# Performance work log

Measured on AMD Instinct MI355X. Metric: run time of the kernel, lower is better.

The kernel has to match this reference:

```python
import jax, jax.numpy as jnp
import numpy as np

N, E = 50000, 500000
HID, H, D = 128, 8, 16
ED, EGD = 32, 64


def _ln(x, g, b):
    m = x.mean(-1, keepdims=True)
    v = ((x - m) ** 2).mean(-1, keepdims=True)
    return (x - m) / jnp.sqrt(v + 1e-5) * g + b


def _gelu(x):
    return jax.nn.gelu(x, approximate=False)  # torch nn.GELU default (erf)


def setup_inputs() -> dict:
    key = jax.random.key(0)
    ks = jax.random.split(key, 24)
    s = lambda k, shape, scale=0.05: jax.random.normal(k, shape, jnp.float32) * scale
    inp = {
        "x": jax.random.normal(ks[0], (N, HID), jnp.float32),
        "edge_attr": jax.random.normal(ks[1], (E, ED), jnp.float32),
        "gamma": jax.random.uniform(ks[2], (N, HID), jnp.float32),
        "beta": jax.random.normal(ks[3], (N, HID), jnp.float32) * 0.1,
        "Wq": s(ks[4], (HID, H * D)),
        "Wk": s(ks[5], (HID, H * D)),
        "Wv": s(ks[6], (HID, H * D)),
        "Wo": s(ks[7], (H * D, HID)),
        "bo": jnp.zeros((HID,), jnp.float32),
        "ea_w1": s(ks[8], (ED, EGD)), "ea_b1": jnp.zeros((EGD,), jnp.float32),
        "ea_w2": s(ks[9], (EGD, H)), "ea_b2": jnp.zeros((H,), jnp.float32),
        "eg_w1": s(ks[10], (ED, EGD)), "eg_b1": jnp.zeros((EGD,), jnp.float32),
        "eg_w2": s(ks[11], (EGD, H * D)), "eg_b2": jnp.zeros((H * D,), jnp.float32),
        "ln1_g": jnp.ones((HID,), jnp.float32), "ln1_b": jnp.zeros((HID,), jnp.float32),
        "ln2_g": jnp.ones((HID,), jnp.float32), "ln2_b": jnp.zeros((HID,), jnp.float32),
        "ffn_w1": s(ks[12], (HID, 2 * HID)), "ffn_b1": jnp.zeros((2 * HID,), jnp.float32),
        "ffn_w2": s(ks[13], (2 * HID, HID)), "ffn_b2": jnp.zeros((HID,), jnp.float32),
        "edge_index": jax.random.randint(ks[14], (2, E), 0, N, jnp.int32),
    }
    return inp


def reference(x, edge_attr, gamma, beta, Wq, Wk, Wv, Wo, bo,
              ea_w1, ea_b1, ea_w2, ea_b2, eg_w1, eg_b1, eg_w2, eg_b2,
              ln1_g, ln1_b, ln2_g, ln2_b, ffn_w1, ffn_b1, ffn_w2, ffn_b2,
              edge_index):
    n = x.shape[0]
    src, dst = edge_index[0], edge_index[1]
    xn = _ln(x, ln1_g, ln1_b)
    Q = (xn @ Wq).reshape(n, H, D)
    K = (xn @ Wk).reshape(n, H, D)
    V = (xn @ Wv).reshape(n, H, D)
    # per-edge attention logits [E, H]
    logits = (Q[dst] * K[src]).sum(-1) * (D ** -0.5)
    logits = logits + (_gelu(edge_attr @ ea_w1 + ea_b1) @ ea_w2 + ea_b2)
    # sparse softmax over edges sharing a destination; torch version
    # initializes max buffer to zeros (include_self), so clamp max at 0
    m = jnp.maximum(jax.ops.segment_max(logits, dst, num_segments=n), 0.0)
    ex = jnp.exp(logits - m[dst])
    ssum = jax.ops.segment_sum(ex, dst, num_segments=n)
    attn = ex / (ssum[dst] + 1e-10)
    gate = jax.nn.sigmoid(_gelu(edge_attr @ eg_w1 + eg_b1) @ eg_w2 + eg_b2).reshape(-1, H, D)
    weighted = attn[..., None] * (gate * V[src])  # [E, H, D]
    agg = jax.ops.segment_sum(weighted, dst, num_segments=n).reshape(n, H * D)
    out = agg @ Wo + bo
    out = gamma * out + beta
    x = x + out
    x2 = _ln(x, ln2_g, ln2_b)
    f = _gelu(x2 @ ffn_w1 + ffn_b1) @ ffn_w2 + ffn_b2
    return x + f
```

## Files before the change

kernel.cpp:

```cpp
#include <hip/hip_runtime.h>

constexpr int N   = 50000;
constexpr int E   = 500000;
constexpr int HID = 128;
constexpr int NH  = 8;
constexpr int ED  = 32;
constexpr int EGD = 64;
constexpr int NB  = (N + 255) / 256;

typedef short  bf16x8 __attribute__((ext_vector_type(8)));
typedef float  f32x4  __attribute__((ext_vector_type(4)));

__device__ __forceinline__ float gelu_f(float v) {
    float u = v * v;
    float a = v * fmaf(u, -0.07135481283f, -1.5957691216f);
    float e = __expf(a);
    return v * __builtin_amdgcn_rcpf(1.f + e);
}
__device__ __forceinline__ float sigm_f(float v) {
    float e = __expf(-v);
    return __builtin_amdgcn_rcpf(1.f + e);
}
__device__ __forceinline__ unsigned short f2bf(float f) {
    unsigned int u = __float_as_uint(f);
    return (unsigned short)((u + 0x7fffu + ((u >> 16) & 1u)) >> 16);
}
__device__ __forceinline__ unsigned int cvt_pk_bf16(float lo, float hi) {
    unsigned int r;
    asm("v_cvt_pk_bf16_f32 %0, %1, %2" : "=v"(r) : "v"(lo), "v"(hi));
    return r;
}
__device__ __forceinline__ float dot2(unsigned int a, unsigned int b) {
    float al = __uint_as_float(a << 16), ah = __uint_as_float(a & 0xffff0000u);
    float bl = __uint_as_float(b << 16), bh = __uint_as_float(b & 0xffff0000u);
    return al * bl + ah * bh;
}

__global__ __launch_bounds__(256) void k_cvt(
    const float* __restrict__ Wq, const float* __restrict__ Wk,
    const float* __restrict__ Wv, const float* __restrict__ Wo,
    const float* __restrict__ fw1, const float* __restrict__ fw2,
    const float* __restrict__ ea_w1, const float* __restrict__ ea_w2,
    const float* __restrict__ eg_w1, const float* __restrict__ eg_w2,
    unsigned short* __restrict__ dst)
{
    int f = blockIdx.x * 256 + threadIdx.x;
    if (f >= 18048) return;
    const float* W; int KT, srcN, base;
    if      (f < 2048)  { W = Wq;    KT = 4; srcN = 128; base = 0; }
    else if (f < 4096)  { W = Wk;    KT = 4; srcN = 128; base = 2048; }
    else if (f < 6144)  { W = Wv;    KT = 4; srcN = 128; base = 4096; }
    else if (f < 8192)  { W = Wo;    KT = 4; srcN = 128; base = 6144; }
    else if (f < 12288) { W = fw1;   KT = 4; srcN = 256; base = 8192; }
    else if (f < 16384) { W = fw2;   KT = 8; srcN = 128; base = 12288; }
    else if (f < 16640) { W = ea_w1; KT = 1; srcN = 64;  base = 16384; }
    else if (f < 16768) { W = ea_w2; KT = 2; srcN = 8;   base = 16640; }
    else if (f < 17024) { W = eg_w1; KT = 1; srcN = 64;  base = 16768; }
    else                { W = eg_w2; KT = 2; srcN = 128; base = 17024; }
    int fl = f - base, lane = fl & 63, t = fl >> 6;
    int ks = t % KT, nt = t / KT;
    int n  = nt * 16 + (lane & 15);
    int k0 = ks * 32 + (lane >> 4) * 8;
    union { unsigned short u[8]; uint4 v; } o;
#pragma unroll
    for (int j = 0; j < 8; j++)
        o.u[j] = (n < srcN) ? f2bf(W[(size_t)(k0 + j) * srcN + n]) : (unsigned short)0;
    *(uint4*)(dst + (size_t)f * 8) = o.v;
}

__global__ __launch_bounds__(64) void k_ln_qkv_mfma(
    const float* __restrict__ x, const float* __restrict__ g1, const float* __restrict__ b1,
    const unsigned short* __restrict__ wqkv,
    unsigned short* __restrict__ Q, unsigned short* __restrict__ K, unsigned short* __restrict__ V)
{
    __shared__ unsigned short xn_lds[16 * 128];
    const int tid = threadIdx.x;
    const int nodeBase = blockIdx.x * 16;

    {
        int nl = tid >> 2, q = tid & 3;
        int gn = nodeBase + nl; if (gn >= N) gn = N - 1;
        const float4* xp = (const float4*)(x + (size_t)gn * HID + q * 32);
        float xv[32]; float s = 0.f, ss = 0.f;
#pragma unroll
        for (int i = 0; i < 8; i++) {
            float4 t = xp[i];
            xv[4*i] = t.x; xv[4*i+1] = t.y; xv[4*i+2] = t.z; xv[4*i+3] = t.w;
        }
#pragma unroll
        for (int i = 0; i < 32; i++) { s += xv[i]; ss += xv[i] * xv[i]; }
        s += __shfl_xor(s, 1); ss += __shfl_xor(ss, 1);
        s += __shfl_xor(s, 2); ss += __shfl_xor(ss, 2);
        float mean = s * (1.f / HID);
        float ri = rsqrtf(ss * (1.f / HID) - mean * mean + 1e-5f);
#pragma unroll
        for (int j = 0; j < 4; j++) {
            union { unsigned short u[8]; uint4 v4; } o;
#pragma unroll
            for (int c = 0; c < 8; c++) {
                int col = q * 32 + j * 8 + c;
                o.u[c] = f2bf((xv[j*8+c] - mean) * ri * g1[col] + b1[col]);
            }
            int phys = (q * 4 + j) ^ (nl & 15);
            *(uint4*)&xn_lds[nl * 128 + phys * 8] = o.v4;
        }
    }

    const int lane = tid, lm = lane & 15, kb = lane >> 4, rowq = kb * 4;
    bf16x8 af[4];
#pragma unroll
    for (int ks = 0; ks < 4; ks++)
        af[ks] = *(const bf16x8*)&xn_lds[lm * 128 + ((ks * 4 + kb) ^ lm) * 8];

    const int node = nodeBase + lm;
    for (int nt = 0; nt < 24; nt++) {
        f32x4 c = {0.f, 0.f, 0.f, 0.f};
#pragma unroll
        for (int ks = 0; ks < 4; ks++)
            c = __builtin_amdgcn_mfma_f32_16x16x32_bf16(
                    *(const bf16x8*)&wqkv[((size_t)(nt * 4 + ks) * 64 + lane) * 8],
                    af[ks], c, 0, 0, 0);
        unsigned short* O = (nt < 8) ? Q : ((nt < 16) ? K : V);
        uint2 o;
        o.x = (unsigned int)f2bf(c[0]) | ((unsigned int)f2bf(c[1]) << 16);
        o.y = (unsigned int)f2bf(c[2]) | ((unsigned int)f2bf(c[3]) << 16);
        *(uint2*)(O + (size_t)node * HID + (nt & 7) * 16 + rowq) = o;
    }
}

__global__ __launch_bounds__(256) void k_hist(const int* __restrict__ ei, int* __restrict__ cnt) {
    int e = blockIdx.x * 256 + threadIdx.x;
    if (e < E) atomicAdd(&cnt[ei[E + e]], 1);
}

__global__ __launch_bounds__(256) void k_bsum(const int* __restrict__ cnt, int* __restrict__ bsum) {
    int i = blockIdx.x * 256 + threadIdx.x;
    int v = (i < N) ? cnt[i] : 0;
#pragma unroll
    for (int m = 1; m < 64; m <<= 1) v += __shfl_xor(v, m);
    __shared__ int ws4[4];
    if ((threadIdx.x & 63) == 0) ws4[threadIdx.x >> 6] = v;
    __syncthreads();
    if (threadIdx.x == 0) bsum[blockIdx.x] = ws4[0] + ws4[1] + ws4[2] + ws4[3];
}

__global__ __launch_bounds__(256) void k_scan_b(const int* __restrict__ bsum, int* __restrict__ boff) {
    __shared__ int s[256];
    int t = threadIdx.x;
    int v = (t < NB) ? bsum[t] : 0;
    s[t] = v; __syncthreads();
    for (int off = 1; off < 256; off <<= 1) {
        int add = (t >= off) ? s[t - off] : 0;
        __syncthreads();
        s[t] += add;
        __syncthreads();
    }
    if (t < NB) boff[t] = s[t] - v;
}

__global__ __launch_bounds__(256) void k_scan_final(
    const int* __restrict__ cnt, const int* __restrict__ boff,
    int* __restrict__ starts, int* __restrict__ cursor)
{
    __shared__ int s[256];
    int t = threadIdx.x, i = blockIdx.x * 256 + t;
    int v = (i < N) ? cnt[i] : 0;
    s[t] = v; __syncthreads();
    for (int off = 1; off < 256; off <<= 1) {
        int add = (t >= off) ? s[t - off] : 0;
        __syncthreads();
        s[t] += add;
        __syncthreads();
    }
    int ex = boff[blockIdx.x] + s[t] - v;
    if (i < N) {
        starts[i] = ex;
        cursor[i] = ex;
        if (i == N - 1) starts[N] = ex + v;
    }
}

__global__ __launch_bounds__(256) void k_scatter(
    const int* __restrict__ ei, int* __restrict__ cursor, uint4* __restrict__ esd)
{
    int e = blockIdx.x * 256 + threadIdx.x;
    if (e < E) {
        int src = ei[e], dst = ei[E + e];
        int p = atomicAdd(&cursor[dst], 1);
        esd[p] = make_uint4((unsigned)src, (unsigned)dst, (unsigned)e, 0u);
    }
}

__global__ __launch_bounds__(256) void k_edge(
    const int bOff,
    const float* __restrict__ edge_attr, const uint4* __restrict__ esd,
    const unsigned short* __restrict__ Qb, const unsigned short* __restrict__ Kb,
    const unsigned short* __restrict__ Vb,
    const unsigned short* __restrict__ w1ea, const float* __restrict__ b1ea,
    const unsigned short* __restrict__ w2ea, const float* __restrict__ b2ea,
    const unsigned short* __restrict__ w1eg, const float* __restrict__ b1eg,
    const unsigned short* __restrict__ w2eg, const float* __restrict__ b2eg,
    float* __restrict__ logit_s, unsigned int* __restrict__ gv)
{
    __shared__ unsigned short ea_lds[256 * 32];
    __shared__ unsigned short sc_lds[4 * 16 * 64];
    __shared__ int perm_lds[256];
    __shared__ int src_lds[256];
    float* st16 = (float*)ea_lds;

    const int tid   = threadIdx.x;
    const int jBase = (blockIdx.x + bOff) * 256;
    const int lane  = tid & 63;
    const int wv    = tid >> 6;
    const int wBase = wv * 64;
    const int lm    = lane & 15;
    const int kb    = lane >> 4;
    const int rowq  = kb * 4;

    const int j  = jBase + tid;
    const int jj = (j < E) ? j : E - 1;
    const uint4 r4 = esd[jj];
    {
        perm_lds[tid] = (int)r4.z;
        src_lds[tid]  = (int)r4.x;
    }
    __syncthreads();

#pragma unroll
    for (int it = 0; it < 8; it++) {
        int idx = it * 256 + tid;
        int el = idx >> 3, c = (idx & 7) * 4;
        int ge = perm_lds[el];
        float4 v = *(const float4*)(edge_attr + (size_t)ge * ED + c);
        int g = ((c >> 3) ^ (el & 3));
        unsigned int lo = (unsigned int)f2bf(v.x) | ((unsigned int)f2bf(v.y) << 16);
        unsigned int hi = (unsigned int)f2bf(v.z) | ((unsigned int)f2bf(v.w) << 16);
        *(uint2*)&ea_lds[el * 32 + g * 8 + (c & 7)] = make_uint2(lo, hi);
    }
    __syncthreads();

    unsigned short* sc = &sc_lds[wv * 1024];

#pragma unroll 1
    for (int et = 0; et < 4; et++) {
        const int am = wBase + et * 16 + lm;
        const bf16x8 a1 = *(const bf16x8*)&ea_lds[am * 32 + (kb ^ (am & 3)) * 8];

        {
            f32x4 acc[4];
#pragma unroll
            for (int nt = 0; nt < 4; nt++) {
                f32x4 z = {0.f, 0.f, 0.f, 0.f};
                acc[nt] = __builtin_amdgcn_mfma_f32_16x16x32_bf16(
                    a1, *(const bf16x8*)&w1ea[(nt * 64 + lane) * 8], z, 0, 0, 0);
            }
#pragma unroll
            for (int nt = 0; nt < 4; nt++) {
                float bias = b1ea[nt * 16 + lm];
#pragma unroll
                for (int r = 0; r < 4; r++) {
                    int el = rowq + r;
                    int kg = nt * 2 + (lm >> 3);
                    sc[el * 64 + ((kg ^ (el & 7)) * 8) + (lm & 7)] =
                        f2bf(gelu_f(acc[nt][r] + bias));
                }
            }
        }
        {
            bf16x8 f0 = *(const bf16x8*)&sc[lm * 64 + ((kb ^ (lm & 7)) * 8)];
            bf16x8 f1 = *(const bf16x8*)&sc[lm * 64 + (((4 + kb) ^ (lm & 7)) * 8)];
            float bias = b2ea[lm & 7];
            f32x4 acc = {bias, bias, bias, bias};
            acc = __builtin_amdgcn_mfma_f32_16x16x32_bf16(
                f0, *(const bf16x8*)&w2ea[(0 * 64 + lane) * 8], acc, 0, 0, 0);
            acc = __builtin_amdgcn_mfma_f32_16x16x32_bf16(
                f1, *(const bf16x8*)&w2ea[(1 * 64 + lane) * 8], acc, 0, 0, 0);
            if (lm < 8) {
#pragma unroll
                for (int r = 0; r < 4; r++)
                    st16[(wBase + et * 16 + rowq + r) * 16 + lm] = acc[r];
            }
        }
        {
            f32x4 acc[4];
#pragma unroll
            for (int nt = 0; nt < 4; nt++) {
                f32x4 z = {0.f, 0.f, 0.f, 0.f};
                acc[nt] = __builtin_amdgcn_mfma_f32_16x16x32_bf16(
                    a1, *(const bf16x8*)&w1eg[(nt * 64 + lane) * 8], z, 0, 0, 0);
            }
#pragma unroll
            for (int nt = 0; nt < 4; nt++) {
                float bias = b1eg[nt * 16 + lm];
#pragma unroll
                for (int r = 0; r < 4; r++) {
                    int el = rowq + r;
                    int kg = nt * 2 + (lm >> 3);
                    sc[el * 64 + ((kg ^ (el & 7)) * 8) + (lm & 7)] =
                        f2bf(gelu_f(acc[nt][r] + bias));
                }
            }
        }
        {
            bf16x8 h0 = *(const bf16x8*)&sc[lm * 64 + ((kb ^ (lm & 7)) * 8)];
            bf16x8 h1 = *(const bf16x8*)&sc[lm * 64 + (((4 + kb) ^ (lm & 7)) * 8)];
            const int e   = jBase + wBase + et * 16 + lm;
            const int src = src_lds[wBase + et * 16 + lm];
            const unsigned short* vrow = Vb + (size_t)src * HID;
            const bool ok = (e < E);
            unsigned int* gvo = gv + (size_t)e * 64 + kb * 2;
#pragma unroll
            for (int mt = 0; mt < 8; mt++) {
                float4 b4 = *(const float4*)&b2eg[mt * 16 + rowq];
                f32x4 acc = {b4.x, b4.y, b4.z, b4.w};
                acc = __builtin_amdgcn_mfma_f32_16x16x32_bf16(
                    *(const bf16x8*)&w2eg[((mt * 2 + 0) * 64 + lane) * 8], h0, acc, 0, 0, 0);
                acc = __builtin_amdgcn_mfma_f32_16x16x32_bf16(
                    *(const bf16x8*)&w2eg[((mt * 2 + 1) * 64 + lane) * 8], h1, acc, 0, 0, 0);
                uint2 vv = *(const uint2*)(vrow + mt * 16 + rowq);
                float w0 = sigm_f(acc[0]) * __uint_as_float(vv.x << 16);
                float w1 = sigm_f(acc[1]) * __uint_as_float(vv.x & 0xffff0000u);
                float w2 = sigm_f(acc[2]) * __uint_as_float(vv.y << 16);
                float w3 = sigm_f(acc[3]) * __uint_as_float(vv.y & 0xffff0000u);
                uint2 o;
                o.x = (unsigned int)f2bf(w0) | ((unsigned int)f2bf(w1) << 16);
                o.y = (unsigned int)f2bf(w2) | ((unsigned int)f2bf(w3) << 16);
                if (ok) *(uint2*)(gvo + mt * 8) = o;
            }
        }
    }

    {
        if (j < E) {
            int src = (int)r4.x, dst = (int)r4.y;
            const uint4* qp = (const uint4*)(Qb + (size_t)dst * HID);
            const uint4* kp = (const uint4*)(Kb + (size_t)src * HID);
            float lg[8];
#pragma unroll
            for (int h = 0; h < 8; h++) {
                float dot = 0.f;
#pragma unroll
                for (int t = 0; t < 2; t++) {
                    uint4 q = qp[h * 2 + t], k4 = kp[h * 2 + t];
                    dot += dot2(q.x, k4.x) + dot2(q.y, k4.y) + dot2(q.z, k4.z) + dot2(q.w, k4.w);
                }
                lg[h] = __expf(fminf(st16[tid * 16 + h] + 0.25f * dot, 80.f));
            }
            float4* op = (float4*)(logit_s + (size_t)j * NH);
            op[0] = make_float4(lg[0], lg[1], lg[2], lg[3]);
            op[1] = make_float4(lg[4], lg[5], lg[6], lg[7]);
        }
    }
}

__global__ __launch_bounds__(256) void k_agg2(
    const int* __restrict__ starts, const unsigned int* __restrict__ gv,
    const float* __restrict__ logit_s, float* __restrict__ agg)
{
    int wave = threadIdx.x >> 6, lane = threadIdx.x & 63;
    int dst = blockIdx.x * 4 + wave;
    if (dst >= N) return;
    int s0 = starts[dst], s1 = starts[dst + 1];
    int head = lane >> 3;
    float ssum = 0.f, ax = 0.f, ay = 0.f;
#pragma unroll 4
    for (int j = s0; j < s1; j++) {
        float e = logit_s[(size_t)j * NH + head];
        unsigned int u = gv[(size_t)j * 64 + lane];
        ssum += e;
        ax += e * __uint_as_float(u << 16);
        ay += e * __uint_as_float(u & 0xffff0000u);
    }
    float rs = __builtin_amdgcn_rcpf(ssum + 1e-10f);
    float2* o = (float2*)(agg + (size_t)dst * HID + lane * 2);
    *o = make_float2(ax * rs, ay * rs);
}

__global__ __launch_bounds__(64) void k_node_out_mfma(
    const float* __restrict__ x, const float* __restrict__ gamma, const float* __restrict__ beta,
    const unsigned short* __restrict__ wo_f, const float* __restrict__ bo,
    const float* __restrict__ g2, const float* __restrict__ b2,
    const unsigned short* __restrict__ fw1_f, const float* __restrict__ fb1,
    const unsigned short* __restrict__ fw2_f, const float* __restrict__ fb2,
    const float* __restrict__ agg, float* __restrict__ out)
{
    __shared__ unsigned short a_lds[16 * 128];
    __shared__ unsigned short f1_lds[16 * 256];
    const int tid = threadIdx.x;
    const int nodeBase = blockIdx.x * 16;

    {
        int nl = tid >> 2, q = tid & 3;
        int gn = nodeBase + nl; if (gn >= N) gn = N - 1;
        const float4* ap = (const float4*)(agg + (size_t)gn * HID + q * 32);
#pragma unroll
        for (int j = 0; j < 4; j++) {
            float4 t0 = ap[2 * j], t1 = ap[2 * j + 1];
            uint4 o;
            o.x = cvt_pk_bf16(t0.x, t0.y); o.y = cvt_pk_bf16(t0.z, t0.w);
            o.z = cvt_pk_bf16(t1.x, t1.y); o.w = cvt_pk_bf16(t1.z, t1.w);
            int phys = (q * 4 + j) ^ (nl & 15);
            *(uint4*)&a_lds[nl * 128 + phys * 8] = o;
        }
    }

    const int lane = tid, lm = lane & 15, kb = lane >> 4;

    f32x4 xo[8];
    {
        bf16x8 af[4];
#pragma unroll
        for (int ks = 0; ks < 4; ks++)
            af[ks] = *(const bf16x8*)&a_lds[lm * 128 + ((ks * 4 + kb) ^ lm) * 8];
#pragma unroll
        for (int nt = 0; nt < 8; nt++) {
            f32x4 c = {0.f, 0.f, 0.f, 0.f};
#pragma unroll
            for (int ks = 0; ks < 4; ks++)
                c = __builtin_amdgcn_mfma_f32_16x16x32_bf16(
                        af[ks], *(const bf16x8*)&wo_f[((size_t)(nt * 4 + ks) * 64 + lane) * 8],
                        c, 0, 0, 0);
            xo[nt] = c;
        }
    }

    float x1v[8][4];
#pragma unroll
    for (int nt = 0; nt < 8; nt++) {
        int col = nt * 16 + lm;
        float boc = bo[col];
#pragma unroll
        for (int r = 0; r < 4; r++) {
            int node = nodeBase + kb * 4 + r; if (node >= N) node = N - 1;
            size_t idx = (size_t)node * HID + col;
            x1v[nt][r] = x[idx] + gamma[idx] * (xo[nt][r] + boc) + beta[idx];
        }
    }

    float s4[4] = {0,0,0,0}, q4[4] = {0,0,0,0};
#pragma unroll
    for (int nt = 0; nt < 8; nt++)
#pragma unroll
        for (int r = 0; r < 4; r++) { s4[r] += x1v[nt][r]; q4[r] += x1v[nt][r] * x1v[nt][r]; }
#pragma unroll
    for (int m = 1; m < 16; m <<= 1)
#pragma unroll
        for (int r = 0; r < 4; r++) { s4[r] += __shfl_xor(s4[r], m); q4[r] += __shfl_xor(q4[r], m); }
    float mu4[4], ri4[4];
#pragma unroll
    for (int r = 0; r < 4; r++) {
        float mu = s4[r] * (1.f / HID);
        mu4[r] = mu;
        ri4[r] = rsqrtf(q4[r] * (1.f / HID) - mu * mu + 1e-5f);
    }

#pragma unroll
    for (int nt = 0; nt < 8; nt++) {
        int col = nt * 16 + lm;
        float g2c = g2[col], b2c = b2[col];
#pragma unroll
        for (int r = 0; r < 4; r++) {
            float xn = (x1v[nt][r] - mu4[r]) * ri4[r] * g2c + b2c;
            int row = kb * 4 + r;
            int g = col >> 3;
            a_lds[row * 128 + (g ^ (row & 15)) * 8 + (col & 7)] = f2bf(xn);
        }
    }

    {
        bf16x8 af[4];
#pragma unroll
        for (int ks = 0; ks < 4; ks++)
            af[ks] = *(const bf16x8*)&a_lds[lm * 128 + ((ks * 4 + kb) ^ lm) * 8];
#pragma unroll
        for (int nt = 0; nt < 16; nt++) {
            f32x4 c = {0.f, 0.f, 0.f, 0.f};
#pragma unroll
            for (int ks = 0; ks < 4; ks++)
                c = __builtin_amdgcn_mfma_f32_16x16x32_bf16(
                        af[ks], *(const bf16x8*)&fw1_f[((size_t)(nt * 4 + ks) * 64 + lane) * 8],
                        c, 0, 0, 0);
            int col = nt * 16 + lm;
            float fbc = fb1[col];
#pragma unroll
            for (int r = 0; r < 4; r++) {
                int row = kb * 4 + r;
                int g = col >> 3;
                int phys = (g & 16) | ((g ^ (row & 15)) & 15);
                f1_lds[row * 256 + phys * 8 + (col & 7)] = f2bf(gelu_f(c[r] + fbc));
            }
        }
    }

    {
        bf16x8 af[8];
#pragma unroll
        for (int ks = 0; ks < 8; ks++) {
            int g = ks * 4 + kb;
            int phys = (g & 16) | ((g ^ lm) & 15);
            af[ks] = *(const bf16x8*)&f1_lds[lm * 256 + phys * 8];
        }
#pragma unroll
        for (int nt = 0; nt < 8; nt++) {
            f32x4 c = {0.f, 0.f, 0.f, 0.f};
#pragma unroll
            for (int ks = 0; ks < 8; ks++)
                c = __builtin_amdgcn_mfma_f32_16x16x32_bf16(
                        af[ks], *(const bf16x8*)&fw2_f[((size_t)(nt * 8 + ks) * 64 + lane) * 8],
                        c, 0, 0, 0);
            int col = nt * 16 + lm;
            float fbc = fb2[col];
#pragma unroll
            for (int r = 0; r < 4; r++) {
                int node = nodeBase + kb * 4 + r;
                if (node < N) out[(size_t)node * HID + col] = x1v[nt][r] + c[r] + fbc;
            }
        }
    }
}

extern "C" void kernel_launch(void* const* d_in, const int* in_sizes, int n_in,
                              void* d_out, int out_size, void* d_ws, size_t ws_size,
                              hipStream_t stream)
{
    const float* x         = (const float*)d_in[0];
    const float* edge_attr = (const float*)d_in[1];
    const float* gamma     = (const float*)d_in[2];
    const float* beta      = (const float*)d_in[3];
    const float* Wq        = (const float*)d_in[4];
    const float* Wk        = (const float*)d_in[5];
    const float* Wv        = (const float*)d_in[6];
    const float* Wo        = (const float*)d_in[7];
    const float* bo        = (const float*)d_in[8];
    const float* ea_w1     = (const float*)d_in[9];
    const float* ea_b1     = (const float*)d_in[10];
    const float* ea_w2     = (const float*)d_in[11];
    const float* ea_b2     = (const float*)d_in[12];
    const float* eg_w1     = (const float*)d_in[13];
    const float* eg_b1     = (const float*)d_in[14];
    const float* eg_w2     = (const float*)d_in[15];
    const float* eg_b2     = (const float*)d_in[16];
    const float* ln1_g     = (const float*)d_in[17];
    const float* ln1_b     = (const float*)d_in[18];
    const float* ln2_g     = (const float*)d_in[19];
    const float* ln2_b     = (const float*)d_in[20];
    const float* fw1       = (const float*)d_in[21];
    const float* fb1       = (const float*)d_in[22];
    const float* fw2       = (const float*)d_in[23];
    const float* fb2       = (const float*)d_in[24];
    const int*   ei        = (const int*)d_in[25];

    char* wsb = (char*)d_ws;
    size_t off = 0;
    auto alloc = [&](size_t bytes) { void* p = wsb + off; off += (bytes + 255) & ~(size_t)255; return p; };

    unsigned short* Qb = (unsigned short*)alloc((size_t)N * HID * 2);
    unsigned short* Kb = (unsigned short*)alloc((size_t)N * HID * 2);
    unsigned short* Vb = (unsigned short*)alloc((size_t)N * HID * 2);
    float* logit_s = (float*)alloc((size_t)E * NH * 4);
    float* aggb    = (float*)alloc((size_t)N * HID * 4);
    int*   cnt     = (int*)alloc((size_t)N * 4);
    int*   starts  = (int*)alloc((size_t)(N + 1) * 4);
    int*   cursor  = (int*)alloc((size_t)N * 4);
    int*   bsum    = (int*)alloc((size_t)NB * 4);
    int*   boff    = (int*)alloc((size_t)NB * 4);
    uint4* esd     = (uint4*)alloc((size_t)E * 16);
    unsigned int*   gvb   = (unsigned int*)alloc((size_t)E * 64 * 4);
    unsigned short* fragW = (unsigned short*)alloc((size_t)18048 * 8 * 2);
    float* outp = (float*)d_out;

    unsigned short* wqkv_f = fragW;
    unsigned short* wo_f   = fragW + (size_t)6144  * 8;
    unsigned short* fw1_f  = fragW + (size_t)8192  * 8;
    unsigned short* fw2_f  = fragW + (size_t)12288 * 8;
    unsigned short* w1ea_f = fragW + (size_t)16384 * 8;
    unsigned short* w2ea_f = fragW + (size_t)16640 * 8;
    unsigned short* w1eg_f = fragW + (size_t)16768 * 8;
    unsigned short* w2eg_f = fragW + (size_t)17024 * 8;

    hipMemsetAsync(cnt, 0, (size_t)N * sizeof(int), stream);

    const int EB = (E + 255) / 256;
    const int NBLK16 = (N + 15) / 16;
    k_cvt<<<(18048 + 255) / 256, 256, 0, stream>>>(Wq, Wk, Wv, Wo, fw1, fw2,
                                                   ea_w1, ea_w2, eg_w1, eg_w2, fragW);
    k_ln_qkv_mfma<<<NBLK16, 64, 0, stream>>>(x, ln1_g, ln1_b, wqkv_f, Qb, Kb, Vb);
    k_hist<<<EB, 256, 0, stream>>>(ei, cnt);
    k_bsum<<<NB, 256, 0, stream>>>(cnt, bsum);
    k_scan_b<<<1, 256, 0, stream>>>(bsum, boff);
    k_scan_final<<<NB, 256, 0, stream>>>(cnt, boff, starts, cursor);
    k_scatter<<<EB, 256, 0, stream>>>(ei, cursor, esd);
    const int C1 = (EB + 1) / 2;
    const int C2 = EB - C1;
    k_edge<<<C1, 256, 0, stream>>>(0,  edge_attr, esd, Qb, Kb, Vb,
                                   w1ea_f, ea_b1, w2ea_f, ea_b2,
                                   w1eg_f, eg_b1, w2eg_f, eg_b2, logit_s, gvb);
    k_edge<<<C2, 256, 0, stream>>>(C1, edge_attr, esd, Qb, Kb, Vb,
                                   w1ea_f, ea_b1, w2ea_f, ea_b2,
                                   w1eg_f, eg_b1, w2eg_f, eg_b2, logit_s, gvb);
    k_agg2<<<(N + 3) / 4, 256, 0, stream>>>(starts, gvb, logit_s, aggb);
    k_node_out_mfma<<<NBLK16, 64, 0, stream>>>(x, gamma, beta, wo_f, bo, ln2_g, ln2_b,
                                               fw1_f, fb1, fw2_f, fb2, aggb, outp);
}
```

Baseline: 532.8 us.

## Split node MFMA kernels across four waves per 16-node block

The LN+QKV and node-output kernels go from one 64-thread wave per 16-node tile to 256 threads. The LDS staging and output N-tiles are split across four waves, and LayerNorm-2 statistics are combined through a small LDS buffer with extra barriers. This shortens the serial MFMA chain per wave and adds parallelism for latency hiding, at the cost of block-level syncs. The two-launch split of the edge kernel is also merged into one launch, and the N-boundary clamps are dropped, which relies on N being divisible by 16.

```diff
diff --git a/kernel.cpp b/kernel.cpp
--- a/kernel.cpp
+++ b/kernel.cpp
@@ -24,11 +24,6 @@
 __device__ __forceinline__ unsigned short f2bf(float f) {
     unsigned int u = __float_as_uint(f);
     return (unsigned short)((u + 0x7fffu + ((u >> 16) & 1u)) >> 16);
-}
-__device__ __forceinline__ unsigned int cvt_pk_bf16(float lo, float hi) {
-    unsigned int r;
-    asm("v_cvt_pk_bf16_f32 %0, %1, %2" : "=v"(r) : "v"(lo), "v"(hi));
-    return r;
 }
 __device__ __forceinline__ float dot2(unsigned int a, unsigned int b) {
     float al = __uint_as_float(a << 16), ah = __uint_as_float(a & 0xffff0000u);
@@ -68,7 +63,7 @@
     *(uint4*)(dst + (size_t)f * 8) = o.v;
 }
 
-__global__ __launch_bounds__(64) void k_ln_qkv_mfma(
+__global__ __launch_bounds__(256) void k_ln_qkv_mfma(
     const float* __restrict__ x, const float* __restrict__ g1, const float* __restrict__ b1,
     const unsigned short* __restrict__ wqkv,
     unsigned short* __restrict__ Q, unsigned short* __restrict__ K, unsigned short* __restrict__ V)
@@ -78,42 +73,40 @@
     const int nodeBase = blockIdx.x * 16;
 
     {
-        int nl = tid >> 2, q = tid & 3;
-        int gn = nodeBase + nl; if (gn >= N) gn = N - 1;
-        const float4* xp = (const float4*)(x + (size_t)gn * HID + q * 32);
-        float xv[32]; float s = 0.f, ss = 0.f;
-#pragma unroll
-        for (int i = 0; i < 8; i++) {
-            float4 t = xp[i];
-            xv[4*i] = t.x; xv[4*i+1] = t.y; xv[4*i+2] = t.z; xv[4*i+3] = t.w;
-        }
-#pragma unroll
-        for (int i = 0; i < 32; i++) { s += xv[i]; ss += xv[i] * xv[i]; }
+        int nl = tid >> 4, q = tid & 15;
+        const float4* xp = (const float4*)(x + (size_t)(nodeBase + nl) * HID + q * 8);
+        float4 t0 = xp[0], t1 = xp[1];
+        float v[8] = {t0.x, t0.y, t0.z, t0.w, t1.x, t1.y, t1.z, t1.w};
+        float s = 0.f, ss = 0.f;
+#pragma unroll
+        for (int i = 0; i < 8; i++) { s += v[i]; ss += v[i] * v[i]; }
         s += __shfl_xor(s, 1); ss += __shfl_xor(ss, 1);
         s += __shfl_xor(s, 2); ss += __shfl_xor(ss, 2);
+        s += __shfl_xor(s, 4); ss += __shfl_xor(ss, 4);
+        s += __shfl_xor(s, 8); ss += __shfl_xor(ss, 8);
         float mean = s * (1.f / HID);
         float ri = rsqrtf(ss * (1.f / HID) - mean * mean + 1e-5f);
-#pragma unroll
-        for (int j = 0; j < 4; j++) {
-            union { unsigned short u[8]; uint4 v4; } o;
-#pragma unroll
-            for (int c = 0; c < 8; c++) {
-                int col = q * 32 + j * 8 + c;
-                o.u[c] = f2bf((xv[j*8+c] - mean) * ri * g1[col] + b1[col]);
-            }
-            int phys = (q * 4 + j) ^ (nl & 15);
-            *(uint4*)&xn_lds[nl * 128 + phys * 8] = o.v4;
-        }
-    }
-
-    const int lane = tid, lm = lane & 15, kb = lane >> 4, rowq = kb * 4;
+        union { unsigned short u[8]; uint4 v4; } o;
+#pragma unroll
+        for (int c = 0; c < 8; c++) {
+            int col = q * 8 + c;
+            o.u[c] = f2bf((v[c] - mean) * ri * g1[col] + b1[col]);
+        }
+        *(uint4*)&xn_lds[nl * 128 + (q ^ nl) * 8] = o.v4;
+    }
+    __syncthreads();
+
+    const int wv = tid >> 6, lane = tid & 63;
+    const int lm = lane & 15, kb = lane >> 4, rowq = kb * 4;
     bf16x8 af[4];
 #pragma unroll
     for (int ks = 0; ks < 4; ks++)
         af[ks] = *(const bf16x8*)&xn_lds[lm * 128 + ((ks * 4 + kb) ^ lm) * 8];
 
     const int node = nodeBase + lm;
-    for (int nt = 0; nt < 24; nt++) {
+#pragma unroll
+    for (int u = 0; u < 6; u++) {
+        int nt = 6 * wv + u;
         f32x4 c = {0.f, 0.f, 0.f, 0.f};
 #pragma unroll
         for (int ks = 0; ks < 4; ks++)
@@ -192,7 +185,6 @@
 }
 
 __global__ __launch_bounds__(256) void k_edge(
-    const int bOff,
     const float* __restrict__ edge_attr, const uint4* __restrict__ esd,
     const unsigned short* __restrict__ Qb, const unsigned short* __restrict__ Kb,
     const unsigned short* __restrict__ Vb,
@@ -209,7 +201,7 @@
     float* st16 = (float*)ea_lds;
 
     const int tid   = threadIdx.x;
-    const int jBase = (blockIdx.x + bOff) * 256;
+    const int jBase = blockIdx.x * 256;
     const int lane  = tid & 63;
     const int wv    = tid >> 6;
     const int wBase = wv * 64;
@@ -376,7 +368,7 @@
     *o = make_float2(ax * rs, ay * rs);
 }
 
-__global__ __launch_bounds__(64) void k_node_out_mfma(
+__global__ __launch_bounds__(256) void k_node_out_mfma(
     const float* __restrict__ x, const float* __restrict__ gamma, const float* __restrict__ beta,
     const unsigned short* __restrict__ wo_f, const float* __restrict__ bo,
     const float* __restrict__ g2, const float* __restrict__ b2,
@@ -386,86 +378,98 @@
 {
     __shared__ unsigned short a_lds[16 * 128];
     __shared__ unsigned short f1_lds[16 * 256];
+    __shared__ float2 sums_lds[16][4];
     const int tid = threadIdx.x;
     const int nodeBase = blockIdx.x * 16;
 
     {
-        int nl = tid >> 2, q = tid & 3;
-        int gn = nodeBase + nl; if (gn >= N) gn = N - 1;
-        const float4* ap = (const float4*)(agg + (size_t)gn * HID + q * 32);
-#pragma unroll
-        for (int j = 0; j < 4; j++) {
-            float4 t0 = ap[2 * j], t1 = ap[2 * j + 1];
-            uint4 o;
-            o.x = cvt_pk_bf16(t0.x, t0.y); o.y = cvt_pk_bf16(t0.z, t0.w);
-            o.z = cvt_pk_bf16(t1.x, t1.y); o.w = cvt_pk_bf16(t1.z, t1.w);
-            int phys = (q * 4 + j) ^ (nl & 15);
-            *(uint4*)&a_lds[nl * 128 + phys * 8] = o;
-        }
-    }
-
-    const int lane = tid, lm = lane & 15, kb = lane >> 4;
-
-    f32x4 xo[8];
+        int nl = tid >> 4, q = tid & 15;
+        const float4* ap = (const float4*)(agg + (size_t)(nodeBase + nl) * HID + q * 8);
+        float4 t0 = ap[0], t1 = ap[1];
+        union { unsigned short u[8]; uint4 v; } o;
+        o.u[0] = f2bf(t0.x); o.u[1] = f2bf(t0.y); o.u[2] = f2bf(t0.z); o.u[3] = f2bf(t0.w);
+        o.u[4] = f2bf(t1.x); o.u[5] = f2bf(t1.y); o.u[6] = f2bf(t1.z); o.u[7] = f2bf(t1.w);
+        *(uint4*)&a_lds[nl * 128 + (q ^ nl) * 8] = o.v;
+    }
+    __syncthreads();
+
+    const int wv = tid >> 6, lane = tid & 63;
+    const int lm = lane & 15, kb = lane >> 4, rowq = kb * 4;
+
+    f32x4 xo[2];
     {
         bf16x8 af[4];
 #pragma unroll
         for (int ks = 0; ks < 4; ks++)
             af[ks] = *(const bf16x8*)&a_lds[lm * 128 + ((ks * 4 + kb) ^ lm) * 8];
 #pragma unroll
-        for (int nt = 0; nt < 8; nt++) {
+        for (int t = 0; t < 2; t++) {
+            int nt = 2 * wv + t;
             f32x4 c = {0.f, 0.f, 0.f, 0.f};
 #pragma unroll
             for (int ks = 0; ks < 4; ks++)
                 c = __builtin_amdgcn_mfma_f32_16x16x32_bf16(
                         af[ks], *(const bf16x8*)&wo_f[((size_t)(nt * 4 + ks) * 64 + lane) * 8],
                         c, 0, 0, 0);
-            xo[nt] = c;
-        }
-    }
-
-    float x1v[8][4];
-#pragma unroll
-    for (int nt = 0; nt < 8; nt++) {
-        int col = nt * 16 + lm;
+            xo[t] = c;
+        }
+    }
+
+    float x1v[2][4];
+#pragma unroll
+    for (int t = 0; t < 2; t++) {
+        int col = (2 * wv + t) * 16 + lm;
         float boc = bo[col];
 #pragma unroll
         for (int r = 0; r < 4; r++) {
-            int node = nodeBase + kb * 4 + r; if (node >= N) node = N - 1;
-            size_t idx = (size_t)node * HID + col;
-            x1v[nt][r] = x[idx] + gamma[idx] * (xo[nt][r] + boc) + beta[idx];
-        }
-    }
-
-    float s4[4] = {0,0,0,0}, q4[4] = {0,0,0,0};
-#pragma unroll
-    for (int nt = 0; nt < 8; nt++)
-#pragma unroll
-        for (int r = 0; r < 4; r++) { s4[r] += x1v[nt][r]; q4[r] += x1v[nt][r] * x1v[nt][r]; }
-#pragma unroll
-    for (int m = 1; m < 16; m <<= 1)
-#pragma unroll
-        for (int r = 0; r < 4; r++) { s4[r] += __shfl_xor(s4[r], m); q4[r] += __shfl_xor(q4[r], m); }
+            size_t idx = (size_t)(nodeBase + rowq + r) * HID + col;
+            x1v[t][r] = x[idx] + gamma[idx] * (xo[t][r] + boc) + beta[idx];
+        }
+    }
+
+    {
+        float s2[4], q2[4];
+#pragma unroll
+        for (int r = 0; r < 4; r++) {
+            s2[r] = x1v[0][r] + x1v[1][r];
+            q2[r] = x1v[0][r] * x1v[0][r] + x1v[1][r] * x1v[1][r];
+        }
+#pragma unroll
+        for (int m = 1; m < 16; m <<= 1)
+#pragma unroll
+            for (int r = 0; r < 4; r++) { s2[r] += __shfl_xor(s2[r], m); q2[r] += __shfl_xor(q2[r], m); }
+        if (lm == 0) {
+#pragma unroll
+            for (int r = 0; r < 4; r++)
+                sums_lds[rowq + r][wv] = make_float2(s2[r], q2[r]);
+        }
+    }
+    __syncthreads();
     float mu4[4], ri4[4];
 #pragma unroll
     for (int r = 0; r < 4; r++) {
-        float mu = s4[r] * (1.f / HID);
+        float2 p0 = sums_lds[rowq + r][0], p1 = sums_lds[rowq + r][1];
+        float2 p2 = sums_lds[rowq + r][2], p3 = sums_lds[rowq + r][3];
+        float s = p0.x + p1.x + p2.x + p3.x;
+        float q = p0.y + p1.y + p2.y + p3.y;
+        float mu = s * (1.f / HID);
         mu4[r] = mu;
-        ri4[r] = rsqrtf(q4[r] * (1.f / HID) - mu * mu + 1e-5f);
-    }
-
-#pragma unroll
-    for (int nt = 0; nt < 8; nt++) {
-        int col = nt * 16 + lm;
+        ri4[r] = rsqrtf(q * (1.f / HID) - mu * mu + 1e-5f);
+    }
+
+#pragma unroll
+    for (int t = 0; t < 2; t++) {
+        int col = (2 * wv + t) * 16 + lm;
         float g2c = g2[col], b2c = b2[col];
 #pragma unroll
         for (int r = 0; r < 4; r++) {
-            float xn = (x1v[nt][r] - mu4[r]) * ri4[r] * g2c + b2c;
-            int row = kb * 4 + r;
+            float xn = (x1v[t][r] - mu4[r]) * ri4[r] * g2c + b2c;
+            int row = rowq + r;
             int g = col >> 3;
-            a_lds[row * 128 + (g ^ (row & 15)) * 8 + (col & 7)] = f2bf(xn);
-        }
-    }
+            a_lds[row * 128 + (g ^ row) * 8 + (col & 7)] = f2bf(xn);
+        }
+    }
+    __syncthreads();
 
     {
         bf16x8 af[4];
@@ -473,7 +477,8 @@
         for (int ks = 0; ks < 4; ks++)
             af[ks] = *(const bf16x8*)&a_lds[lm * 128 + ((ks * 4 + kb) ^ lm) * 8];
 #pragma unroll
-        for (int nt = 0; nt < 16; nt++) {
+        for (int u = 0; u < 4; u++) {
+            int nt = 4 * wv + u;
             f32x4 c = {0.f, 0.f, 0.f, 0.f};
 #pragma unroll
             for (int ks = 0; ks < 4; ks++)
@@ -484,13 +489,14 @@
             float fbc = fb1[col];
 #pragma unroll
             for (int r = 0; r < 4; r++) {
-                int row = kb * 4 + r;
+                int row = rowq + r;
                 int g = col >> 3;
-                int phys = (g & 16) | ((g ^ (row & 15)) & 15);
+                int phys = (g & 16) | ((g ^ row) & 15);
                 f1_lds[row * 256 + phys * 8 + (col & 7)] = f2bf(gelu_f(c[r] + fbc));
             }
         }
     }
+    __syncthreads();
 
     {
         bf16x8 af[8];
@@ -501,7 +507,8 @@
             af[ks] = *(const bf16x8*)&f1_lds[lm * 256 + phys * 8];
         }
 #pragma unroll
-        for (int nt = 0; nt < 8; nt++) {
+        for (int t = 0; t < 2; t++) {
+            int nt = 2 * wv + t;
             f32x4 c = {0.f, 0.f, 0.f, 0.f};
 #pragma unroll
             for (int ks = 0; ks < 8; ks++)
@@ -512,8 +519,8 @@
             float fbc = fb2[col];
 #pragma unroll
             for (int r = 0; r < 4; r++) {
-                int node = nodeBase + kb * 4 + r;
-                if (node < N) out[(size_t)node * HID + col] = x1v[nt][r] + c[r] + fbc;
+                int node = nodeBase + rowq + r;
+                out[(size_t)node * HID + col] = x1v[t][r] + c[r] + fbc;
             }
         }
     }
@@ -584,21 +591,17 @@
     const int NBLK16 = (N + 15) / 16;
     k_cvt<<<(18048 + 255) / 256, 256, 0, stream>>>(Wq, Wk, Wv, Wo, fw1, fw2,
                                                    ea_w1, ea_w2, eg_w1, eg_w2, fragW);
-    k_ln_qkv_mfma<<<NBLK16, 64, 0, stream>>>(x, ln1_g, ln1_b, wqkv_f, Qb, Kb, Vb);
+    k_ln_qkv_mfma<<<NBLK16, 256, 0, stream>>>(x, ln1_g, ln1_b, wqkv_f, Qb, Kb, Vb);
     k_hist<<<EB, 256, 0, stream>>>(ei, cnt);
     k_bsum<<<NB, 256, 0, stream>>>(cnt, bsum);
     k_scan_b<<<1, 256, 0, stream>>>(bsum, boff);
     k_scan_final<<<NB, 256, 0, stream>>>(cnt, boff, starts, cursor);
     k_scatter<<<EB, 256, 0, stream>>>(ei, cursor, esd);
-    const int C1 = (EB + 1) / 2;
-    const int C2 = EB - C1;
-    k_edge<<<C1, 256, 0, stream>>>(0,  edge_attr, esd, Qb, Kb, Vb,
+    k_edge<<<EB, 256, 0, stream>>>(edge_attr, esd, Qb, Kb, Vb,
                                    w1ea_f, ea_b1, w2ea_f, ea_b2,
-                                   w1eg_f, eg_b1, w2eg_f, eg_b2, logit_s, gvb);
-    k_edge<<<C2, 256, 0, stream>>>(C1, edge_attr, esd, Qb, Kb, Vb,
-                                   w1ea_f, ea_b1, w2ea_f, ea_b2,
-                                   w1eg_f, eg_b1, w2eg_f, eg_b2, logit_s, gvb);
+                                   w1eg_f, eg_b1, w2eg_f, eg_b2,
+                                   logit_s, gvb);
     k_agg2<<<(N + 3) / 4, 256, 0, stream>>>(starts, gvb, logit_s, aggb);
-    k_node_out_mfma<<<NBLK16, 64, 0, stream>>>(x, gamma, beta, wo_f, bo, ln2_g, ln2_b,
-                                               fw1_f, fb1, fw2_f, fb2, aggb, outp);
-}
+    k_node_out_mfma<<<NBLK16, 256, 0, stream>>>(x, gamma, beta, wo_f, bo, ln2_g, ln2_b,
+                                                fw1_f, fb1, fw2_f, fb2, aggb, outp);
+}
```

After: 453.2 us. 14.9% less time.
